# Kernel tuning notes

Measured on AMD Instinct MI355X. Metric: run time of the kernel, lower is better.

## Reference

```python
import jax, jax.numpy as jnp
import numpy as np

B, N, D = 8, 4096, 512
NUM_CODES = 8192

def setup_inputs() -> dict:
    key = jax.random.key(0)
    kx, kc = jax.random.split(key)
    x = jax.random.normal(kx, (B, N, D), dtype=jnp.float32)
    codebook = jax.random.normal(kc, (NUM_CODES, D), dtype=jnp.float32)
    return {"x": x, "codebook": codebook}

def reference(x, codebook):
    # x: (B, N, D); codebook: (K, D)
    b = x.shape[0]
    flat = x.reshape(-1, x.shape[-1])  # (B*N, D)
    distances = (
        jnp.sum(flat * flat, axis=1, keepdims=True)
        + jnp.sum(codebook * codebook, axis=1)
        - 2.0 * flat @ codebook.T
    )
    codes = jnp.argmin(distances, axis=1).reshape(b, -1)  # (B, N) int
    return codes
```

## Files before the change

### kernel.cpp

```cpp
#include <hip/hip_runtime.h>
#include <hip/hip_bf16.h>
#include <hip/hip_fp16.h>


#define M_ROWS 32768
#define DDIM   512
#define KCODES 8192
#define NCAND  8

typedef unsigned long long u64;
typedef unsigned int u32;
typedef __attribute__((ext_vector_type(4))) float f32x4;
typedef __attribute__((ext_vector_type(8))) int v8i;

#define GL2LDS(gp, lp) __builtin_amdgcn_global_load_lds(                  \
    (const __attribute__((address_space(1))) void*)(gp),                  \
    (__attribute__((address_space(3))) void*)(lp), 16, 0, 0)

#define WAITV2() asm volatile("s_waitcnt vmcnt(2)" ::: "memory")
#define WAITL()  asm volatile("s_waitcnt lgkmcnt(0)" ::: "memory")
#define SBAR()   __builtin_amdgcn_sched_barrier(0)
#define BAR() do { SBAR(); __builtin_amdgcn_s_barrier(); SBAR(); } while (0)

__device__ __forceinline__ u32 umin32(u32 a, u32 b) { return a < b ? a : b; }
__device__ __forceinline__ u32 umax32(u32 a, u32 b) { return a > b ? a : b; }
__device__ __forceinline__ u64 umin64(u64 a, u64 b) { return a < b ? a : b; }
__device__ __forceinline__ u32 umin3(u32 a, u32 b, u32 c) {
  return umin32(umin32(a, b), c);
}
__device__ __forceinline__ u32 med3u(u32 a, u32 b, u32 c) {
  u32 d;
  asm("v_med3_u32 %0, %1, %2, %3" : "=v"(d) : "v"(a), "v"(b), "v"(c));
  return d;
}

__device__ __forceinline__ u32 fsort(float s) {
  u32 fb = __float_as_uint(s);
  return fb ^ (u32)(((int)fb >> 31) | 0x80000000);
}

__device__ __forceinline__ uint2 pk8_fp8(float4 v0, float4 v1) {
  int lo = 0, hi = 0;
  lo = __builtin_amdgcn_cvt_pk_fp8_f32(v0.x, v0.y, lo, false);
  lo = __builtin_amdgcn_cvt_pk_fp8_f32(v0.z, v0.w, lo, true);
  hi = __builtin_amdgcn_cvt_pk_fp8_f32(v1.x, v1.y, hi, false);
  hi = __builtin_amdgcn_cvt_pk_fp8_f32(v1.z, v1.w, hi, true);
  return (uint2){(u32)lo, (u32)hi};
}

__global__ __launch_bounds__(256) void conv_codebook_kernel(
    const float* __restrict__ cb, unsigned char* __restrict__ ch8,
    float* __restrict__ cnh) {
  int wave = (blockIdx.x * 256 + threadIdx.x) >> 6;
  int lane = threadIdx.x & 63;
  if (wave >= KCODES) return;
  const float* src = cb + (size_t)wave * DDIM + lane * 8;
  float4 v0 = *(const float4*)(src);
  float4 v1 = *(const float4*)(src + 4);
  *(uint2*)(ch8 + (size_t)wave * DDIM + lane * 8) = pk8_fp8(v0, v1);
  float ss = v0.x*v0.x + v0.y*v0.y + v0.z*v0.z + v0.w*v0.w
           + v1.x*v1.x + v1.y*v1.y + v1.z*v1.z + v1.w*v1.w;
#pragma unroll
  for (int off = 32; off; off >>= 1) ss += __shfl_xor(ss, off);
  if (lane == 0) cnh[wave] = 0.5f * ss;
}

__global__ __launch_bounds__(256) void conv_x_kernel(
    const float* __restrict__ x, unsigned char* __restrict__ xh8) {
  size_t i = ((size_t)blockIdx.x * 256 + threadIdx.x) * 8;
  float4 v0 = *(const float4*)(x + i);
  float4 v1 = *(const float4*)(x + i + 4);
  *(uint2*)(xh8 + i) = pk8_fp8(v0, v1);
}

__global__ __launch_bounds__(512, 4) void coarse_kernel(
    const unsigned char* __restrict__ xh8, const unsigned char* __restrict__ ch8,
    const float* __restrict__ cnh, uint4* __restrict__ part) {
  __shared__ __align__(16) char smem[46080];
  float* cnL = (float*)(smem + 24576);
  uint2* tab = (uint2*)(smem + 28672);

  const int tid  = threadIdx.x;
  const int lane = tid & 63;
  const int wid  = tid >> 6;
  const int wm   = wid >> 1, wn = wid & 1;
  const int g    = lane >> 4, l16 = lane & 15;

  const int mblk = blockIdx.x >> 3;
  const int ngrp = blockIdx.x & 7;
  const int row0 = mblk * 128;
  const int colgrp = ngrp * 1024;

  v8i A[2][4];
#pragma unroll
  for (int tm = 0; tm < 2; ++tm) {
    const unsigned char* ap =
        xh8 + (size_t)(row0 + wm * 32 + tm * 16 + l16) * DDIM + g * 32;
#pragma unroll
    for (int c = 0; c < 4; ++c) {
      int4 lo = *(const int4*)(ap + c * 128);
      int4 hi = *(const int4*)(ap + c * 128 + 16);
      A[tm][c][0] = lo.x; A[tm][c][1] = lo.y; A[tm][c][2] = lo.z; A[tm][c][3] = lo.w;
      A[tm][c][4] = hi.x; A[tm][c][5] = hi.y; A[tm][c][6] = hi.z; A[tm][c][7] = hi.w;
    }
  }

  if (tid < 256)
    *(float4*)(cnL + tid * 4) = *(const float4*)(cnh + colgrp + tid * 4);

  const int scode = tid >> 3;
  const int sgran = (tid & 7) ^ (scode & 7);
  const unsigned char* bsrc =
      ch8 + (size_t)(colgrp + scode) * DDIM + sgran * 16;
  char* ldst = smem + tid * 16;

  const int boff = (wn * 32 + l16) * 128 + (((g * 2) ^ (l16 & 7)) << 4);

  u32 m1 = ~0u, m2 = ~0u, m3 = ~0u;

  SBAR();
  GL2LDS(bsrc +   0, ldst);
  GL2LDS(bsrc + 128, ldst + 8192);
  GL2LDS(bsrc + 256, ldst + 16384);
  SBAR();
  WAITL();

  int bsel = 0;
  for (int nb = 0; nb < 16; ++nb) {
    f32x4 acc[2][2];
#pragma unroll
    for (int tm = 0; tm < 2; ++tm)
#pragma unroll
      for (int tn = 0; tn < 2; ++tn) acc[tm][tn] = (f32x4){0.f, 0.f, 0.f, 0.f};

#pragma unroll
    for (int c = 0; c < 4; ++c) {
      int rb = bsel + c; if (rb >= 3) rb -= 3;
      WAITV2();
      BAR();
      const char* bL = smem + rb * 8192;
#pragma unroll
      for (int tn = 0; tn < 2; ++tn) {
        int4 lo = *(const int4*)(bL + boff + tn * 2048);
        int4 hi = *(const int4*)(bL + ((boff + tn * 2048) ^ 16));
        v8i bf;
        bf[0] = lo.x; bf[1] = lo.y; bf[2] = lo.z; bf[3] = lo.w;
        bf[4] = hi.x; bf[5] = hi.y; bf[6] = hi.z; bf[7] = hi.w;
#pragma unroll
        for (int tm = 0; tm < 2; ++tm)
          acc[tm][tn] = __builtin_amdgcn_mfma_scale_f32_16x16x128_f8f6f4(
              A[tm][c], bf, acc[tm][tn],
              0, 0,
              0, 0x7F7F7F7F,
              0, 0x7F7F7F7F);
      }
      WAITL();
      BAR();
      GL2LDS(bsrc + (c == 0 ? 384 : 32768 + (c - 1) * 128), ldst + rb * 8192);
      SBAR();
    }

    const int col0 = colgrp + nb * 64;
#pragma unroll
    for (int p = 0; p < 2; ++p) {
      if (wn == p) {
        u32 codev[2];
        float cnv[2];
#pragma unroll
        for (int tn = 0; tn < 2; ++tn) {
          codev[tn] = (u32)(col0 + wn * 32 + tn * 16 + l16);
          cnv[tn] = cnL[nb * 64 + wn * 32 + tn * 16 + l16];
        }
#pragma unroll
        for (int tm = 0; tm < 2; ++tm)
#pragma unroll
          for (int r = 0; r < 4; ++r) {
            float s0 = cnv[0] - acc[tm][0][r];
            float s1 = cnv[1] - acc[tm][1][r];
            u32 key0 = (__float_as_uint(s0) & 0xFFFFE000u) | codev[0];
            u32 key1 = (__float_as_uint(s1) & 0xFFFFE000u) | codev[1];
            const int row = wm * 32 + tm * 16 + g * 4 + r;
            tab[row * 17 + l16] = (uint2){umin32(key0, key1), umax32(key0, key1)};
          }
      }
      WAITL();
      BAR();
      if (tid < 128) {
#pragma unroll
        for (int e = 0; e < 16; ++e) {
          uint2 v = tab[tid * 17 + e];
          u32 a = umax32(m1, v.x);
          m1 = umin32(m1, v.x);
          u32 b = med3u(m2, a, v.y);
          m2 = umin3(m2, a, v.y);
          m3 = umin32(m3, b);
        }
      }
      BAR();
    }

    if ((nb & 3) == 3) {
      if (tid < 128) {
        part[(size_t)(ngrp * 4 + (nb >> 2)) * M_ROWS + row0 + tid] =
            (uint4){m1, m2, m3, 0u};
        m1 = ~0u; m2 = ~0u; m3 = ~0u;
      }
    }
    bsrc += 32768;
    bsel = (bsel == 2) ? 0 : bsel + 1;
  }
}

__global__ __launch_bounds__(256) void merge_kernel(
    const uint4* __restrict__ part, int* __restrict__ cand) {
  const int row = blockIdx.x * 256 + threadIdx.x;
  u32 k[NCAND];
#pragma unroll
  for (int i = 0; i < NCAND; ++i) k[i] = ~0u;
  for (int nb = 0; nb < KCODES / 256; ++nb) {
    uint4 e = part[(size_t)nb * M_ROWS + row];
    u32 t = e.x;
#pragma unroll
    for (int i = 0; i < NCAND; ++i) { u32 mx = umax32(k[i], t); k[i] = umin32(k[i], t); t = mx; }
    t = e.y;
#pragma unroll
    for (int i = 0; i < NCAND; ++i) { u32 mx = umax32(k[i], t); k[i] = umin32(k[i], t); t = mx; }
    t = e.z;
#pragma unroll
    for (int i = 0; i < NCAND; ++i) { u32 mx = umax32(k[i], t); k[i] = umin32(k[i], t); t = mx; }
  }
#pragma unroll
  for (int i = 0; i < NCAND; ++i)
    cand[row * NCAND + i] = (int)(k[i] & 0x1FFFu);
}

__global__ __launch_bounds__(256) void rescore_kernel(
    const float* __restrict__ x, const float* __restrict__ cb,
    const float* __restrict__ cnh, const int* __restrict__ cand,
    int* __restrict__ out) {
  int wave = (blockIdx.x * 256 + threadIdx.x) >> 6;
  int lane = threadIdx.x & 63;
  if (wave >= M_ROWS) return;
  int idx[NCAND];
#pragma unroll
  for (int j = 0; j < NCAND; ++j) idx[j] = cand[wave * NCAND + j];

  const float* xr = x + (size_t)wave * DDIM + lane * 8;
  float4 x0 = *(const float4*)(xr);
  float4 x1 = *(const float4*)(xr + 4);

  float d[NCAND];
#pragma unroll
  for (int j = 0; j < NCAND; ++j) {
    const float* c = cb + (size_t)idx[j] * DDIM + lane * 8;
    float4 a0 = *(const float4*)(c);
    float4 a1 = *(const float4*)(c + 4);
    d[j] = x0.x*a0.x + x0.y*a0.y + x0.z*a0.z + x0.w*a0.w
         + x1.x*a1.x + x1.y*a1.y + x1.z*a1.z + x1.w*a1.w;
  }
#pragma unroll
  for (int off = 32; off; off >>= 1)
#pragma unroll
    for (int j = 0; j < NCAND; ++j) d[j] += __shfl_xor(d[j], off);

  if (lane == 0) {
    u64 best = ~0ull;
#pragma unroll
    for (int j = 0; j < NCAND; ++j) {
      float s = cnh[idx[j]] - d[j];
      u64 key = ((u64)fsort(s) << 32) | (u32)idx[j];
      best = umin64(best, key);
    }
    out[wave] = (int)(u32)best;
  }
}

extern "C" void kernel_launch(void* const* d_in, const int* in_sizes, int n_in,
                              void* d_out, int out_size, void* d_ws, size_t ws_size,
                              hipStream_t stream) {
  const float* x  = (const float*)d_in[0];
  const float* cb = (const float*)d_in[1];
  int* out = (int*)d_out;

  char* ws = (char*)d_ws;
  unsigned char* ch8  = (unsigned char*)(ws);
  unsigned char* xh8  = (unsigned char*)(ws + (size_t)4 * 1024 * 1024);
  float*         cnh  = (float*)(ws + (size_t)20 * 1024 * 1024);
  int*           cand = (int*)(ws + (size_t)20 * 1024 * 1024 + 32 * 1024);
  uint4*         part = (uint4*)(ws + (size_t)22 * 1024 * 1024);

  conv_codebook_kernel<<<KCODES / 4, 256, 0, stream>>>(cb, ch8, cnh);
  conv_x_kernel<<<(M_ROWS * DDIM) / (256 * 8), 256, 0, stream>>>(x, xh8);
  coarse_kernel<<<(M_ROWS / 128) * 8, 512, 0, stream>>>(xh8, ch8, cnh, part);
  merge_kernel<<<M_ROWS / 256, 256, 0, stream>>>(part, cand);
  rescore_kernel<<<M_ROWS / 4, 256, 0, stream>>>(x, cb, cnh, cand, out);
}
```

Before: 374.6 us.

## Halve coarse-kernel block to 256 threads with 64-row per-wave register tiles

The coarse FP8 MFMA kernel now runs 4 waves per block instead of 8. Each wave computes 64 rows by 32 codes (four row tiles), so every B fragment read from LDS feeds four MFMAs instead of two, and each thread issues two global-to-LDS copies per stage. The wait count is raised to match the doubled number of outstanding loads, and waves-per-EU is pinned to 2 to allow the larger A and accumulator register footprint. In exchange there are fewer resident waves to hide latency, and register pressure rises.

After: 391.1 us. +4.4%, slower.

```diff
diff --git a/kernel.cpp b/kernel.cpp
--- a/kernel.cpp
+++ b/kernel.cpp
@@ -17,7 +17,7 @@
     (const __attribute__((address_space(1))) void*)(gp),                  \
     (__attribute__((address_space(3))) void*)(lp), 16, 0, 0)
 
-#define WAITV2() asm volatile("s_waitcnt vmcnt(2)" ::: "memory")
+#define WAITV4() asm volatile("s_waitcnt vmcnt(4)" ::: "memory")
 #define WAITL()  asm volatile("s_waitcnt lgkmcnt(0)" ::: "memory")
 #define SBAR()   __builtin_amdgcn_sched_barrier(0)
 #define BAR() do { SBAR(); __builtin_amdgcn_s_barrier(); SBAR(); } while (0)
@@ -73,7 +73,9 @@
   *(uint2*)(xh8 + i) = pk8_fp8(v0, v1);
 }
 
-__global__ __launch_bounds__(512, 4) void coarse_kernel(
+__global__ __launch_bounds__(256)
+__attribute__((amdgpu_waves_per_eu(2, 2)))
+void coarse_kernel(
     const unsigned char* __restrict__ xh8, const unsigned char* __restrict__ ch8,
     const float* __restrict__ cnh, uint4* __restrict__ part) {
   __shared__ __align__(16) char smem[46080];
@@ -91,11 +93,11 @@
   const int row0 = mblk * 128;
   const int colgrp = ngrp * 1024;
 
-  v8i A[2][4];
-#pragma unroll
-  for (int tm = 0; tm < 2; ++tm) {
+  v8i A[4][4];
+#pragma unroll
+  for (int tm = 0; tm < 4; ++tm) {
     const unsigned char* ap =
-        xh8 + (size_t)(row0 + wm * 32 + tm * 16 + l16) * DDIM + g * 32;
+        xh8 + (size_t)(row0 + wm * 64 + tm * 16 + l16) * DDIM + g * 32;
 #pragma unroll
     for (int c = 0; c < 4; ++c) {
       int4 lo = *(const int4*)(ap + c * 128);
@@ -105,13 +107,13 @@
     }
   }
 
-  if (tid < 256)
-    *(float4*)(cnL + tid * 4) = *(const float4*)(cnh + colgrp + tid * 4);
-
-  const int scode = tid >> 3;
-  const int sgran = (tid & 7) ^ (scode & 7);
-  const unsigned char* bsrc =
-      ch8 + (size_t)(colgrp + scode) * DDIM + sgran * 16;
+  *(float4*)(cnL + tid * 4) = *(const float4*)(cnh + colgrp + tid * 4);
+
+  const int sc1 = tid >> 3;
+  const int sl  = tid & 7;
+  const unsigned char* bsrc1 =
+      ch8 + (size_t)(colgrp + sc1) * DDIM + ((sl ^ (sc1 & 7)) << 4);
+  const unsigned char* bsrc2 = bsrc1 + (size_t)32 * DDIM;
   char* ldst = smem + tid * 16;
 
   const int boff = (wn * 32 + l16) * 128 + (((g * 2) ^ (l16 & 7)) << 4);
@@ -119,24 +121,24 @@
   u32 m1 = ~0u, m2 = ~0u, m3 = ~0u;
 
   SBAR();
-  GL2LDS(bsrc +   0, ldst);
-  GL2LDS(bsrc + 128, ldst + 8192);
-  GL2LDS(bsrc + 256, ldst + 16384);
+  GL2LDS(bsrc1 +   0, ldst);          GL2LDS(bsrc2 +   0, ldst + 4096);
+  GL2LDS(bsrc1 + 128, ldst +  8192);  GL2LDS(bsrc2 + 128, ldst + 12288);
+  GL2LDS(bsrc1 + 256, ldst + 16384);  GL2LDS(bsrc2 + 256, ldst + 20480);
   SBAR();
   WAITL();
 
   int bsel = 0;
   for (int nb = 0; nb < 16; ++nb) {
-    f32x4 acc[2][2];
-#pragma unroll
-    for (int tm = 0; tm < 2; ++tm)
+    f32x4 acc[4][2];
+#pragma unroll
+    for (int tm = 0; tm < 4; ++tm)
 #pragma unroll
       for (int tn = 0; tn < 2; ++tn) acc[tm][tn] = (f32x4){0.f, 0.f, 0.f, 0.f};
 
 #pragma unroll
     for (int c = 0; c < 4; ++c) {
       int rb = bsel + c; if (rb >= 3) rb -= 3;
-      WAITV2();
+      WAITV4();
       BAR();
       const char* bL = smem + rb * 8192;
 #pragma unroll
@@ -147,7 +149,7 @@
         bf[0] = lo.x; bf[1] = lo.y; bf[2] = lo.z; bf[3] = lo.w;
         bf[4] = hi.x; bf[5] = hi.y; bf[6] = hi.z; bf[7] = hi.w;
 #pragma unroll
-        for (int tm = 0; tm < 2; ++tm)
+        for (int tm = 0; tm < 4; ++tm)
           acc[tm][tn] = __builtin_amdgcn_mfma_scale_f32_16x16x128_f8f6f4(
               A[tm][c], bf, acc[tm][tn],
               0, 0,
@@ -156,7 +158,11 @@
       }
       WAITL();
       BAR();
-      GL2LDS(bsrc + (c == 0 ? 384 : 32768 + (c - 1) * 128), ldst + rb * 8192);
+      {
+        const int koff = (c == 0 ? 384 : 32768 + (c - 1) * 128);
+        GL2LDS(bsrc1 + koff, ldst + rb * 8192);
+        GL2LDS(bsrc2 + koff, ldst + rb * 8192 + 4096);
+      }
       SBAR();
     }
 
@@ -172,14 +178,14 @@
           cnv[tn] = cnL[nb * 64 + wn * 32 + tn * 16 + l16];
         }
 #pragma unroll
-        for (int tm = 0; tm < 2; ++tm)
+        for (int tm = 0; tm < 4; ++tm)
 #pragma unroll
           for (int r = 0; r < 4; ++r) {
             float s0 = cnv[0] - acc[tm][0][r];
             float s1 = cnv[1] - acc[tm][1][r];
             u32 key0 = (__float_as_uint(s0) & 0xFFFFE000u) | codev[0];
             u32 key1 = (__float_as_uint(s1) & 0xFFFFE000u) | codev[1];
-            const int row = wm * 32 + tm * 16 + g * 4 + r;
+            const int row = wm * 64 + tm * 16 + g * 4 + r;
             tab[row * 17 + l16] = (uint2){umin32(key0, key1), umax32(key0, key1)};
           }
       }
@@ -206,7 +212,8 @@
         m1 = ~0u; m2 = ~0u; m3 = ~0u;
       }
     }
-    bsrc += 32768;
+    bsrc1 += 32768;
+    bsrc2 += 32768;
     bsel = (bsel == 2) ? 0 : bsel + 1;
   }
 }
@@ -291,7 +298,7 @@
 
   conv_codebook_kernel<<<KCODES / 4, 256, 0, stream>>>(cb, ch8, cnh);
   conv_x_kernel<<<(M_ROWS * DDIM) / (256 * 8), 256, 0, stream>>>(x, xh8);
-  coarse_kernel<<<(M_ROWS / 128) * 8, 512, 0, stream>>>(xh8, ch8, cnh, part);
+  coarse_kernel<<<(M_ROWS / 128) * 8, 256, 0, stream>>>(xh8, ch8, cnh, part);
   merge_kernel<<<M_ROWS / 256, 256, 0, stream>>>(part, cand);
   rescore_kernel<<<M_ROWS / 4, 256, 0, stream>>>(x, cb, cnh, cand, out);
 }
```
